# Kernel tuning notes

Hardware: AMD Instinct MI355X
Metric: run time of the kernel (lower is better)

Reference implementation:

```python
import jax, jax.numpy as jnp
import numpy as np

NUM_CLASSES = 1000
TEMPERATURE = 0.1
B, B_OOD, D = 4096, 4096, 512


def _l2norm(x):
    return x / jnp.linalg.norm(x, axis=-1, keepdims=True)


def setup_inputs() -> dict:
    key = jax.random.key(0)
    k1, k2, k3, k4, k5 = jax.random.split(key, 5)
    return {
        "centers1": _l2norm(jax.random.normal(k1, (NUM_CLASSES, D), dtype=jnp.float32)),
        "features": _l2norm(jax.random.normal(k2, (B, D), dtype=jnp.float32)),
        "targets": jax.random.randint(k3, (B,), 0, NUM_CLASSES, dtype=jnp.int64 if jax.config.jax_enable_x64 else jnp.int32),
        "features_ood": _l2norm(jax.random.normal(k4, (B_OOD, D), dtype=jnp.float32)),
        "pseudo_target_ood": jax.random.randint(k5, (B_OOD,), 0, NUM_CLASSES, dtype=jnp.int64 if jax.config.jax_enable_x64 else jnp.int32),
    }


def reference(centers1, features, targets, features_ood, pseudo_target_ood):
    C = centers1.shape[0]
    b = features.shape[0]
    bo = features_ood.shape[0]
    n = b + C + bo  # total anchors: batch + class centers + ood

    centers_lbl = jnp.arange(C, dtype=targets.dtype)
    ood_lbl = jnp.full((bo,), C, dtype=targets.dtype)  # ood gets label == num_classes
    targets_all = jnp.concatenate([targets, centers_lbl, ood_lbl])              # [N]
    targets_all_class = jnp.concatenate([targets, centers_lbl, pseudo_target_ood])  # [N]

    # per-class count over all N labels (pseudo labels for ood)
    batch_cls_count = jnp.zeros((C,), dtype=jnp.float32).at[targets_all_class].add(1.0)

    # positive mask: same label as anchor, excluding self (diagonal for j < B)
    mask = (targets_all[:b, None] == targets_all[None, :]).astype(jnp.float32)  # [B,N]
    logits_mask = 1.0 - (jnp.arange(n)[None, :] == jnp.arange(b)[:, None]).astype(jnp.float32)
    mask = mask * logits_mask

    features_all = jnp.concatenate([features, centers1, features_ood], axis=0)  # [N,D]
    logits = jnp.matmul(features, features_all.T) / TEMPERATURE                 # [B,N]
    logits = logits - jax.lax.stop_gradient(jnp.max(logits, axis=1, keepdims=True))

    exp_logits = jnp.exp(logits) * logits_mask
    # class-balanced per-instance weight (count of the column's class, minus positive mask)
    per_ins_weight = batch_cls_count[targets_all_class][None, :] - mask         # [B,N]
    exp_logits_sum = jnp.sum(exp_logits / per_ins_weight, axis=1, keepdims=True)
    log_prob = logits - jnp.log(exp_logits_sum)

    mean_log_prob_pos = jnp.sum(mask * log_prob, axis=1) / jnp.sum(mask, axis=1)
    loss = -jnp.mean(mean_log_prob_pos)
    return loss
```

## Files before the change

kernel.cpp:

```cpp
#include <hip/hip_runtime.h>
#include <stdint.h>

#define NUM_C 1000
#define NB    4096
#define NCOL  9192
#define NPAD  9216
#define DK    512
#define BM    128
#define BN    256
#define BKB   32
#define INV_T 10.0f

typedef __attribute__((ext_vector_type(4))) float f32x4;

#define OFF_FALL  0u
#define OFF_CNTP  4718592u
#define OFF_CNTTP 4784128u
#define OFF_S     4849664u
#define OFF_P     4866048u

__device__ __forceinline__ void async16(const void* g, void* l) {
  __builtin_amdgcn_global_load_lds((const __attribute__((address_space(1))) void*)g,
                                   (__attribute__((address_space(3))) void*)l,
                                   16, 0, 0);
}

__device__ __forceinline__ unsigned sw_e4m3(float x) {
  float ax = fabsf(x);
  unsigned s = (__float_as_uint(x) >> 24) & 0x80u;
  if (ax < 0.015625f) {
    int n = (int)rintf(ax * 512.0f);
    if (n >= 8) return s | 0x08u;
    return s | (unsigned)n;
  }
  if (ax >= 448.0f) return s | 0x7Eu;
  unsigned u = __float_as_uint(ax);
  int ee = (int)(u >> 23) - 127;
  float scale = __uint_as_float((unsigned)(3 - ee + 127) << 23);
  int qv = (int)rintf(ax * scale);
  if (qv == 16) { ee++; qv = 8; }
  return s | (unsigned)(((ee + 7) << 3) | (qv - 8));
}

template <bool HI>
__device__ __forceinline__ int cvt2(float a, float b, int old) {
#if __has_builtin(__builtin_amdgcn_cvt_pk_fp8_f32)
  return __builtin_amdgcn_cvt_pk_fp8_f32(a, b, old, HI);
#else
  unsigned pk = sw_e4m3(a) | (sw_e4m3(b) << 8);
  return HI ? (int)(((unsigned)old & 0x0000FFFFu) | (pk << 16))
            : (int)(((unsigned)old & 0xFFFF0000u) | pk);
#endif
}

__global__ __launch_bounds__(256) void prep_k(const float* __restrict__ centers,
                                              const float* __restrict__ feats,
                                              const float* __restrict__ ood,
                                              const int* __restrict__ targets,
                                              const int* __restrict__ pseudo,
                                              unsigned char* __restrict__ fall,
                                              unsigned* __restrict__ cntP,
                                              unsigned* __restrict__ cntTP,
                                              float* __restrict__ SP) {
  __shared__ unsigned hc[1024];
  __shared__ unsigned hct[1024];
  const int tid = threadIdx.x;

  int idx = blockIdx.x * 256 + tid;
  int row = idx >> 5;
  int ck  = (idx & 31) * 16;
  const float* src = nullptr;
  if (row < NB)              src = feats   + (size_t)row * DK + ck;
  else if (row < NB + NUM_C) src = centers + (size_t)(row - NB) * DK + ck;
  else if (row < NCOL)       src = ood     + (size_t)(row - NB - NUM_C) * DK + ck;
  unsigned w[4] = {0u, 0u, 0u, 0u};
  if (src) {
#pragma unroll
    for (int g = 0; g < 4; g++) {
      float4 v0 = *(const float4*)(src + g * 4);
      int p = 0;
      p = cvt2<false>(v0.x, v0.y, p);
      p = cvt2<true>(v0.z, v0.w, p);
      w[g] = (unsigned)p;
    }
  }
  *(uint4*)(fall + (size_t)row * DK + ck) = make_uint4(w[0], w[1], w[2], w[3]);

  if (blockIdx.x < 16) {
    for (int k = tid; k < 1024; k += 256) { hc[k] = 0u; hct[k] = 0u; }
    __syncthreads();
    int i = blockIdx.x * 256 + tid;
    int t = targets[i];
    atomicAdd(&hc[t], 1u);
    atomicAdd(&hct[t], 1u);
    atomicAdd(&hc[pseudo[i]], 1u);
    __syncthreads();
    for (int k = tid; k < 1024; k += 256) {
      cntP[blockIdx.x * 1024 + k]  = hc[k];
      cntTP[blockIdx.x * 1024 + k] = hct[k];
    }
  } else if (blockIdx.x < 48) {
    SP[(blockIdx.x - 16) * 256 + tid] = 0.0f;
  }
}

__global__ __launch_bounds__(256, 2) void gemm_fused(const unsigned char* __restrict__ fall,
                                                     const int* __restrict__ targets,
                                                     const int* __restrict__ pseudo,
                                                     const unsigned* __restrict__ cntP,
                                                     float* __restrict__ Sacc,
                                                     float* __restrict__ Pacc) {
  __shared__ unsigned char As[BM * BKB];
  __shared__ unsigned char Bs[BN * BKB];
  __shared__ int    sLbl[BN];
  __shared__ float  sRw0[BN];
  __shared__ float  sRw1[BN];
  __shared__ int    sTgt[BM];

  const int tid   = threadIdx.x;
  const int nTile = blockIdx.x;
  const int mTile = blockIdx.y;
  const int lane  = tid & 63;
  const int wv    = tid >> 6;
  const int wm    = wv >> 1;
  const int wn    = wv & 1;
  const int q     = lane >> 4;
  const int cIdx  = lane & 15;

  {
    int j = nTile * BN + tid;
    int lbl, tac;
    if (j >= NCOL)         { lbl = -1; tac = -1; }
    else if (j < NB)       { tac = targets[j]; lbl = tac; }
    else if (j < NB+NUM_C) { tac = j - NB;     lbl = tac; }
    else                   { tac = pseudo[j - NB - NUM_C]; lbl = NUM_C; }
    sLbl[tid] = lbl;
    if (tac >= 0) {
      unsigned c = 1u;
#pragma unroll
      for (int b = 0; b < 16; b++) c += cntP[b * 1024 + tac];
      float w = (float)c;
      sRw0[tid] = 1.0f / w;
      sRw1[tid] = 1.0f / (w - 1.0f);
    } else {
      sRw0[tid] = 0.f;
      sRw1[tid] = 0.f;
    }
    if (tid < BM) sTgt[tid] = targets[mTile * BM + tid];
  }

  f32x4 acc[4][8];
#pragma unroll
  for (int mi = 0; mi < 4; mi++)
#pragma unroll
    for (int ni = 0; ni < 8; ni++)
      acc[mi][ni] = (f32x4){0.f, 0.f, 0.f, 0.f};

  const int aRow0 = mTile * BM;
  const int bRow0 = nTile * BN;

  const int sRow = tid >> 1;
  const int cg   = (tid & 1) ^ (sRow & 1);
  const unsigned char* gA  = fall + (size_t)(aRow0 + sRow)       * DK + cg * 16;
  const unsigned char* gB0 = fall + (size_t)(bRow0 + sRow)       * DK + cg * 16;
  const unsigned char* gB1 = fall + (size_t)(bRow0 + 128 + sRow) * DK + cg * 16;
  unsigned char* lA  = As + tid * 16;
  unsigned char* lB0 = Bs + tid * 16;
  unsigned char* lB1 = Bs + 4096 + tid * 16;

  const int fOff = ((((q >> 1) ^ (cIdx & 1)) << 4) | ((q & 1) << 3));

  for (int kt = 0; kt < DK; kt += BKB) {
    __syncthreads();
    async16(gA + kt, lA);
    async16(gB0 + kt, lB0);
    async16(gB1 + kt, lB1);
    __syncthreads();

    long long af[4];
    long long bf8[8];
#pragma unroll
    for (int mi = 0; mi < 4; mi++)
      af[mi] = *(const long long*)&As[(wm * 64 + mi * 16 + cIdx) * BKB + fOff];
#pragma unroll
    for (int ni = 0; ni < 8; ni++)
      bf8[ni] = *(const long long*)&Bs[(wn * 128 + ni * 16 + cIdx) * BKB + fOff];
#pragma unroll
    for (int mi = 0; mi < 4; mi++)
#pragma unroll
      for (int ni = 0; ni < 8; ni++)
        acc[mi][ni] = __builtin_amdgcn_mfma_f32_16x16x32_fp8_fp8(af[mi], bf8[ni], acc[mi][ni], 0, 0, 0);
  }

  float vS[16], vP[16];
#pragma unroll
  for (int s = 0; s < 16; s++) { vS[s] = 0.f; vP[s] = 0.f; }

#pragma unroll
  for (int ni = 0; ni < 8; ni++) {
    int jloc = wn * 128 + ni * 16 + cIdx;
    int j    = nTile * BN + jloc;
    int lblj = sLbl[jloc];
    float rw0 = sRw0[jloc], rw1 = sRw1[jloc];
#pragma unroll
    for (int mi = 0; mi < 4; mi++) {
      f32x4 a = acc[mi][ni];
#pragma unroll
      for (int r = 0; r < 4; r++) {
        int iloc = wm * 64 + mi * 16 + q * 4 + r;
        int i    = mTile * BM + iloc;
        int ti   = sTgt[iloc];
        float l  = a[r] * INV_T;
        bool diag = (j == i);
        bool pos  = (lblj == ti) && !diag;
        float rw  = diag ? 0.0f : (pos ? rw1 : rw0);
        float e   = __expf(l - 10.0f) * rw;
        vS[mi * 4 + r] += e;
        vP[mi * 4 + r] += pos ? l : 0.0f;
      }
    }
  }

#define RED_STEP(m, s, h)                                        \
  {                                                              \
    float sendS = (cIdx & (m)) ? vS[(s)] : vS[(s) + (h)];        \
    float sendP = (cIdx & (m)) ? vP[(s)] : vP[(s) + (h)];        \
    float rS = __shfl_xor(sendS, (m), 64);                       \
    float rP = __shfl_xor(sendP, (m), 64);                       \
    vS[(s)] = ((cIdx & (m)) ? vS[(s) + (h)] : vS[(s)]) + rS;     \
    vP[(s)] = ((cIdx & (m)) ? vP[(s) + (h)] : vP[(s)]) + rP;     \
  }
  RED_STEP(8, 0, 8) RED_STEP(8, 1, 8) RED_STEP(8, 2, 8) RED_STEP(8, 3, 8)
  RED_STEP(8, 4, 8) RED_STEP(8, 5, 8) RED_STEP(8, 6, 8) RED_STEP(8, 7, 8)
  RED_STEP(4, 0, 4) RED_STEP(4, 1, 4) RED_STEP(4, 2, 4) RED_STEP(4, 3, 4)
  RED_STEP(2, 0, 2) RED_STEP(2, 1, 2)
  RED_STEP(1, 0, 1)
#undef RED_STEP

  {
    int rowLoc = wm * 64 + (cIdx >> 2) * 16 + q * 4 + (cIdx & 3);
    int i = mTile * BM + rowLoc;
    atomicAdd(&Sacc[i], vS[0]);
    atomicAdd(&Pacc[i], vP[0]);
  }
}

__global__ __launch_bounds__(256) void finalize_k(const float* __restrict__ S,
                                                  const float* __restrict__ P,
                                                  const int* __restrict__ targets,
                                                  const unsigned* __restrict__ cntTP,
                                                  float* __restrict__ out) {
  __shared__ unsigned ct[1024];
  __shared__ float red[4];
  int tid = threadIdx.x;
  for (int k = tid; k < 1024; k += 256) {
    unsigned c = 0u;
#pragma unroll
    for (int b = 0; b < 16; b++) c += cntTP[b * 1024 + k];
    ct[k] = c;
  }
  __syncthreads();
  float local = 0.f;
  for (int i = tid; i < NB; i += 256) {
    float npos = (float)ct[targets[i]];
    local += P[i] / npos - INV_T - __logf(S[i]);
  }
  for (int m = 1; m < 64; m <<= 1) local += __shfl_xor(local, m, 64);
  if ((tid & 63) == 0) red[tid >> 6] = local;
  __syncthreads();
  if (tid == 0) {
    float t = red[0] + red[1] + red[2] + red[3];
    out[0] = -t / (float)NB;
  }
}

extern "C" void kernel_launch(void* const* d_in, const int* in_sizes, int n_in,
                              void* d_out, int out_size, void* d_ws, size_t ws_size,
                              hipStream_t stream) {
  const float* centers = (const float*)d_in[0];
  const float* feats   = (const float*)d_in[1];
  const int*   targets = (const int*)d_in[2];
  const float* ood     = (const float*)d_in[3];
  const int*   pseudo  = (const int*)d_in[4];

  char* ws = (char*)d_ws;
  unsigned char* fall  = (unsigned char*)(ws + OFF_FALL);
  unsigned*      cntP  = (unsigned*)(ws + OFF_CNTP);
  unsigned*      cntTP = (unsigned*)(ws + OFF_CNTTP);
  float*         Sacc  = (float*)(ws + OFF_S);
  float*         Pacc  = (float*)(ws + OFF_P);

  prep_k<<<dim3((NPAD * 32) / 256), 256, 0, stream>>>(centers, feats, ood, targets, pseudo,
                                                      fall, cntP, cntTP, Sacc);
  gemm_fused<<<dim3(NPAD / BN, NB / BM), 256, 0, stream>>>(fall, targets, pseudo, cntP, Sacc, Pacc);
  finalize_k<<<1, 256, 0, stream>>>(Sacc, Pacc, targets, cntTP, (float*)d_out);
}
```

Measured before the change: 147.4 us.

## Triple-buffer per-wave private LDS tiles with async loads and no block barriers

Each wave now loads only the A and B slices it needs into its own triple-buffered shared-memory region, issuing async global-to-LDS loads two k-steps ahead. It waits with explicit vmcnt counters instead of two __syncthreads per k-step. The aim is to overlap global loads with MFMA work and remove block-wide barrier stalls in the main loop. The cost is duplicate global/L2 reads, since waves sharing rows or columns each fetch them. It also raises LDS use to about 72 KB per block and drops the previous bank-conflict swizzle.

```diff
diff --git a/kernel.cpp b/kernel.cpp
--- a/kernel.cpp
+++ b/kernel.cpp
@@ -8,7 +8,6 @@
 #define DK    512
 #define BM    128
 #define BN    256
-#define BKB   32
 #define INV_T 10.0f
 
 typedef __attribute__((ext_vector_type(4))) float f32x4;
@@ -110,8 +109,7 @@
                                                      const unsigned* __restrict__ cntP,
                                                      float* __restrict__ Sacc,
                                                      float* __restrict__ Pacc) {
-  __shared__ unsigned char As[BM * BKB];
-  __shared__ unsigned char Bs[BN * BKB];
+  __shared__ unsigned char W[4][3 * 6144];
   __shared__ int    sLbl[BN];
   __shared__ float  sRw0[BN];
   __shared__ float  sRw1[BN];
@@ -126,6 +124,9 @@
   const int wn    = wv & 1;
   const int q     = lane >> 4;
   const int cIdx  = lane & 15;
+
+  const int aRow0 = mTile * BM;
+  const int bRow0 = nTile * BN;
 
   {
     int j = nTile * BN + tid;
@@ -148,6 +149,7 @@
     }
     if (tid < BM) sTgt[tid] = targets[mTile * BM + tid];
   }
+  __syncthreads();
 
   f32x4 acc[4][8];
 #pragma unroll
@@ -156,41 +158,53 @@
     for (int ni = 0; ni < 8; ni++)
       acc[mi][ni] = (f32x4){0.f, 0.f, 0.f, 0.f};
 
-  const int aRow0 = mTile * BM;
-  const int bRow0 = nTile * BN;
-
-  const int sRow = tid >> 1;
-  const int cg   = (tid & 1) ^ (sRow & 1);
-  const unsigned char* gA  = fall + (size_t)(aRow0 + sRow)       * DK + cg * 16;
-  const unsigned char* gB0 = fall + (size_t)(bRow0 + sRow)       * DK + cg * 16;
-  const unsigned char* gB1 = fall + (size_t)(bRow0 + 128 + sRow) * DK + cg * 16;
-  unsigned char* lA  = As + tid * 16;
-  unsigned char* lB0 = Bs + tid * 16;
-  unsigned char* lB1 = Bs + 4096 + tid * 16;
-
-  const int fOff = ((((q >> 1) ^ (cIdx & 1)) << 4) | ((q & 1) << 3));
-
-  for (int kt = 0; kt < DK; kt += BKB) {
-    __syncthreads();
-    async16(gA + kt, lA);
-    async16(gB0 + kt, lB0);
-    async16(gB1 + kt, lB1);
-    __syncthreads();
-
+  const unsigned char* baseA = fall + (size_t)(aRow0 + wm * 64  + (lane >> 1)) * DK + (lane & 1) * 16;
+  const unsigned char* baseB = fall + (size_t)(bRow0 + wn * 128 + (lane >> 1)) * DK + (lane & 1) * 16;
+  unsigned char* lw = &W[wv][0] + lane * 16;
+
+  auto issue = [&](int j, int buf) {
+    const unsigned char* ga = baseA + j * 32;
+    const unsigned char* gb = baseB + j * 32;
+    unsigned char* la = lw + buf * 6144;
+    unsigned char* lb = la + 2048;
+    async16(ga,             la);
+    async16(ga + 32 * DK,   la + 1024);
+    async16(gb,             lb);
+    async16(gb + 32 * DK,   lb + 1024);
+    async16(gb + 64 * DK,   lb + 2048);
+    async16(gb + 96 * DK,   lb + 3072);
+  };
+
+  auto compute = [&](int buf) {
+    const unsigned char* la = &W[wv][buf * 6144];
+    const unsigned char* lb = la + 2048;
     long long af[4];
     long long bf8[8];
 #pragma unroll
     for (int mi = 0; mi < 4; mi++)
-      af[mi] = *(const long long*)&As[(wm * 64 + mi * 16 + cIdx) * BKB + fOff];
+      af[mi] = *(const long long*)(la + (mi * 16 + cIdx) * 32 + q * 8);
 #pragma unroll
     for (int ni = 0; ni < 8; ni++)
-      bf8[ni] = *(const long long*)&Bs[(wn * 128 + ni * 16 + cIdx) * BKB + fOff];
+      bf8[ni] = *(const long long*)(lb + (ni * 16 + cIdx) * 32 + q * 8);
 #pragma unroll
     for (int mi = 0; mi < 4; mi++)
 #pragma unroll
       for (int ni = 0; ni < 8; ni++)
         acc[mi][ni] = __builtin_amdgcn_mfma_f32_16x16x32_fp8_fp8(af[mi], bf8[ni], acc[mi][ni], 0, 0, 0);
-  }
+  };
+
+  issue(0, 0);
+  issue(1, 1);
+#pragma unroll
+  for (int i = 0; i < 14; i++) {
+    asm volatile("s_waitcnt vmcnt(6)" ::: "memory");
+    issue(i + 2, (i + 2) % 3);
+    compute(i % 3);
+  }
+  asm volatile("s_waitcnt vmcnt(6)" ::: "memory");
+  compute(14 % 3);
+  asm volatile("s_waitcnt vmcnt(0)" ::: "memory");
+  compute(15 % 3);
 
   float vS[16], vP[16];
 #pragma unroll
```

Result: faster. 141.4 us (-4.1%).

## Pre-swizzle fp8 features into MFMA fragment layout and load operands directly to registers

Applied to the files above, without the earlier changes.

The prep kernel now writes the fp8-converted features in a per-16-row, per-32-k fragment order that matches the MFMA 16x16x32 operand layout, so each lane's 8-byte fragment is contiguous. The GEMM drops the LDS staging and its two barriers per k-step. It loads A and B fragments straight from global memory into registers, double-buffered with a one-step prefetch. This removes LDS traffic and synchronization, but each wave now re-reads operands from global/L2 with no sharing inside the block, and the extra register buffers may pressure occupancy.

```diff
diff --git a/kernel.cpp b/kernel.cpp
--- a/kernel.cpp
+++ b/kernel.cpp
@@ -8,7 +8,6 @@
 #define DK    512
 #define BM    128
 #define BN    256
-#define BKB   32
 #define INV_T 10.0f
 
 typedef __attribute__((ext_vector_type(4))) float f32x4;
@@ -18,12 +17,6 @@
 #define OFF_CNTTP 4784128u
 #define OFF_S     4849664u
 #define OFF_P     4866048u
-
-__device__ __forceinline__ void async16(const void* g, void* l) {
-  __builtin_amdgcn_global_load_lds((const __attribute__((address_space(1))) void*)g,
-                                   (__attribute__((address_space(3))) void*)l,
-                                   16, 0, 0);
-}
 
 __device__ __forceinline__ unsigned sw_e4m3(float x) {
   float ax = fabsf(x);
@@ -58,7 +51,7 @@
                                               const float* __restrict__ ood,
                                               const int* __restrict__ targets,
                                               const int* __restrict__ pseudo,
-                                              unsigned char* __restrict__ fall,
+                                              unsigned long long* __restrict__ fall,
                                               unsigned* __restrict__ cntP,
                                               unsigned* __restrict__ cntTP,
                                               float* __restrict__ SP) {
@@ -66,28 +59,32 @@
   __shared__ unsigned hct[1024];
   const int tid = threadIdx.x;
 
-  int idx = blockIdx.x * 256 + tid;
-  int row = idx >> 5;
-  int ck  = (idx & 31) * 16;
+  int idx  = blockIdx.x * 256 + tid;
+  int lane = idx & 63;
+  int k32  = (idx >> 6) & 15;
+  int r16  = idx >> 10;
+  int row  = r16 * 16 + (lane & 15);
+  int k    = k32 * 32 + (lane >> 4) * 8;
+
   const float* src = nullptr;
-  if (row < NB)              src = feats   + (size_t)row * DK + ck;
-  else if (row < NB + NUM_C) src = centers + (size_t)(row - NB) * DK + ck;
-  else if (row < NCOL)       src = ood     + (size_t)(row - NB - NUM_C) * DK + ck;
-  unsigned w[4] = {0u, 0u, 0u, 0u};
+  if (row < NB)              src = feats   + (size_t)row * DK + k;
+  else if (row < NB + NUM_C) src = centers + (size_t)(row - NB) * DK + k;
+  else if (row < NCOL)       src = ood     + (size_t)(row - NB - NUM_C) * DK + k;
+  unsigned long long frag = 0ull;
   if (src) {
-#pragma unroll
-    for (int g = 0; g < 4; g++) {
-      float4 v0 = *(const float4*)(src + g * 4);
-      int p = 0;
-      p = cvt2<false>(v0.x, v0.y, p);
-      p = cvt2<true>(v0.z, v0.w, p);
-      w[g] = (unsigned)p;
-    }
-  }
-  *(uint4*)(fall + (size_t)row * DK + ck) = make_uint4(w[0], w[1], w[2], w[3]);
+    float4 v0 = *(const float4*)(src);
+    float4 v1 = *(const float4*)(src + 4);
+    int p0 = 0, p1 = 0;
+    p0 = cvt2<false>(v0.x, v0.y, p0);
+    p0 = cvt2<true>(v0.z, v0.w, p0);
+    p1 = cvt2<false>(v1.x, v1.y, p1);
+    p1 = cvt2<true>(v1.z, v1.w, p1);
+    frag = (unsigned long long)(unsigned)p0 | ((unsigned long long)(unsigned)p1 << 32);
+  }
+  fall[idx] = frag;
 
   if (blockIdx.x < 16) {
-    for (int k = tid; k < 1024; k += 256) { hc[k] = 0u; hct[k] = 0u; }
+    for (int kk = tid; kk < 1024; kk += 256) { hc[kk] = 0u; hct[kk] = 0u; }
     __syncthreads();
     int i = blockIdx.x * 256 + tid;
     int t = targets[i];
@@ -95,9 +92,9 @@
     atomicAdd(&hct[t], 1u);
     atomicAdd(&hc[pseudo[i]], 1u);
     __syncthreads();
-    for (int k = tid; k < 1024; k += 256) {
-      cntP[blockIdx.x * 1024 + k]  = hc[k];
-      cntTP[blockIdx.x * 1024 + k] = hct[k];
+    for (int kk = tid; kk < 1024; kk += 256) {
+      cntP[blockIdx.x * 1024 + kk]  = hc[kk];
+      cntTP[blockIdx.x * 1024 + kk] = hct[kk];
     }
   } else if (blockIdx.x < 48) {
     SP[(blockIdx.x - 16) * 256 + tid] = 0.0f;
@@ -110,8 +107,6 @@
                                                      const unsigned* __restrict__ cntP,
                                                      float* __restrict__ Sacc,
                                                      float* __restrict__ Pacc) {
-  __shared__ unsigned char As[BM * BKB];
-  __shared__ unsigned char Bs[BN * BKB];
   __shared__ int    sLbl[BN];
   __shared__ float  sRw0[BN];
   __shared__ float  sRw1[BN];
@@ -148,6 +143,7 @@
     }
     if (tid < BM) sTgt[tid] = targets[mTile * BM + tid];
   }
+  __syncthreads();
 
   f32x4 acc[4][8];
 #pragma unroll
@@ -156,40 +152,35 @@
     for (int ni = 0; ni < 8; ni++)
       acc[mi][ni] = (f32x4){0.f, 0.f, 0.f, 0.f};
 
-  const int aRow0 = mTile * BM;
-  const int bRow0 = nTile * BN;
-
-  const int sRow = tid >> 1;
-  const int cg   = (tid & 1) ^ (sRow & 1);
-  const unsigned char* gA  = fall + (size_t)(aRow0 + sRow)       * DK + cg * 16;
-  const unsigned char* gB0 = fall + (size_t)(bRow0 + sRow)       * DK + cg * 16;
-  const unsigned char* gB1 = fall + (size_t)(bRow0 + 128 + sRow) * DK + cg * 16;
-  unsigned char* lA  = As + tid * 16;
-  unsigned char* lB0 = Bs + tid * 16;
-  unsigned char* lB1 = Bs + 4096 + tid * 16;
-
-  const int fOff = ((((q >> 1) ^ (cIdx & 1)) << 4) | ((q & 1) << 3));
-
-  for (int kt = 0; kt < DK; kt += BKB) {
-    __syncthreads();
-    async16(gA + kt, lA);
-    async16(gB0 + kt, lB0);
-    async16(gB1 + kt, lB1);
-    __syncthreads();
-
-    long long af[4];
-    long long bf8[8];
+  const unsigned char* aPtr = fall + ((size_t)(mTile * 8 + wm * 4))  * 8192 + lane * 8;
+  const unsigned char* bPtr = fall + ((size_t)(nTile * 16 + wn * 8)) * 8192 + lane * 8;
+
+  long long aCur[4], bCur[8], aNxt[4], bNxt[8];
+#pragma unroll
+  for (int mi = 0; mi < 4; mi++) aCur[mi] = *(const long long*)(aPtr + mi * 8192);
+#pragma unroll
+  for (int ni = 0; ni < 8; ni++) bCur[ni] = *(const long long*)(bPtr + ni * 8192);
+
+#pragma unroll
+  for (int it = 0; it < 16; it++) {
+    if (it < 15) {
+      const int ko = (it + 1) * 512;
+#pragma unroll
+      for (int mi = 0; mi < 4; mi++) aNxt[mi] = *(const long long*)(aPtr + mi * 8192 + ko);
+#pragma unroll
+      for (int ni = 0; ni < 8; ni++) bNxt[ni] = *(const long long*)(bPtr + ni * 8192 + ko);
+    }
 #pragma unroll
     for (int mi = 0; mi < 4; mi++)
-      af[mi] = *(const long long*)&As[(wm * 64 + mi * 16 + cIdx) * BKB + fOff];
-#pragma unroll
-    for (int ni = 0; ni < 8; ni++)
-      bf8[ni] = *(const long long*)&Bs[(wn * 128 + ni * 16 + cIdx) * BKB + fOff];
-#pragma unroll
-    for (int mi = 0; mi < 4; mi++)
 #pragma unroll
       for (int ni = 0; ni < 8; ni++)
-        acc[mi][ni] = __builtin_amdgcn_mfma_f32_16x16x32_fp8_fp8(af[mi], bf8[ni], acc[mi][ni], 0, 0, 0);
+        acc[mi][ni] = __builtin_amdgcn_mfma_f32_16x16x32_fp8_fp8(aCur[mi], bCur[ni], acc[mi][ni], 0, 0, 0);
+    if (it < 15) {
+#pragma unroll
+      for (int mi = 0; mi < 4; mi++) aCur[mi] = aNxt[mi];
+#pragma unroll
+      for (int ni = 0; ni < 8; ni++) bCur[ni] = bNxt[ni];
+    }
   }
 
   float vS[16], vP[16];
@@ -284,14 +275,15 @@
   const int*   pseudo  = (const int*)d_in[4];
 
   char* ws = (char*)d_ws;
-  unsigned char* fall  = (unsigned char*)(ws + OFF_FALL);
-  unsigned*      cntP  = (unsigned*)(ws + OFF_CNTP);
-  unsigned*      cntTP = (unsigned*)(ws + OFF_CNTTP);
-  float*         Sacc  = (float*)(ws + OFF_S);
-  float*         Pacc  = (float*)(ws + OFF_P);
-
-  prep_k<<<dim3((NPAD * 32) / 256), 256, 0, stream>>>(centers, feats, ood, targets, pseudo,
+  unsigned long long* fall  = (unsigned long long*)(ws + OFF_FALL);
+  unsigned*           cntP  = (unsigned*)(ws + OFF_CNTP);
+  unsigned*           cntTP = (unsigned*)(ws + OFF_CNTTP);
+  float*              Sacc  = (float*)(ws + OFF_S);
+  float*              Pacc  = (float*)(ws + OFF_P);
+
+  prep_k<<<dim3((NPAD * 64) / 256), 256, 0, stream>>>(centers, feats, ood, targets, pseudo,
                                                       fall, cntP, cntTP, Sacc);
-  gemm_fused<<<dim3(NPAD / BN, NB / BM), 256, 0, stream>>>(fall, targets, pseudo, cntP, Sacc, Pacc);
+  gemm_fused<<<dim3(NPAD / BN, NB / BM), 256, 0, stream>>>((const unsigned char*)fall, targets,
+                                                           pseudo, cntP, Sacc, Pacc);
   finalize_k<<<1, 256, 0, stream>>>(Sacc, Pacc, targets, cntTP, (float*)d_out);
 }
```

Measured after the change: 130.3 us. 1.13x faster.
